# Kernel tuning notes

Measured on AMD Instinct MI355X. Metric: run time of the kernel, lower is better.

The kernel has to match this reference:

```python
import jax, jax.numpy as jnp
import numpy as np

B, S, D, H = 2, 2048, 2048, 16
HD = D // H  # 128


def setup_inputs() -> dict:
    key = jax.random.key(0)
    ks = jax.random.split(key, 7)
    x = jax.random.normal(ks[0], (B, S, D), jnp.float32)
    # 4 tree-position components per token (e.g. depth/branch coordinates)
    pos = jax.random.uniform(ks[1], (B, S, 4), jnp.float32, 0.0, 64.0)
    # tree/causal additive mask: 0 where attending is allowed, -1e9 otherwise
    causal = jnp.where(jnp.tril(jnp.ones((S, S), bool)), 0.0, -1e9).astype(jnp.float32)
    mask = jnp.broadcast_to(causal, (B, S, S))
    scale = D ** -0.5
    wq = jax.random.normal(ks[2], (D, D), jnp.float32) * scale
    wk = jax.random.normal(ks[3], (D, D), jnp.float32) * scale
    wv = jax.random.normal(ks[4], (D, D), jnp.float32) * scale
    wo = jax.random.normal(ks[5], (D, D), jnp.float32) * scale
    return {"x": x, "pos": pos, "mask": mask, "wq": wq, "wk": wk, "wv": wv, "wo": wo}


def reference(x, pos, mask, wq, wk, wv, wo):
    b, s, d = x.shape
    hd = HD
    # theta_of_dims: 1/10000^(arange(0,hd,8)[:hd//8]/hd) -> [hd//8]
    theta = 1.0 / (10000.0 ** (jnp.arange(0, hd, 8)[: hd // 8].astype(jnp.float32) / hd))
    q = (x @ wq.T).reshape(b, s, H, hd)
    k = (x @ wk.T).reshape(b, s, H, hd)
    v = (x @ wv.T).reshape(b, s, H, hd)
    # freqs: [b, s, hd//8, 4] flattened to [b, s, 1, hd//2]
    freqs = jnp.einsum('bij,k->bikj', pos, theta).reshape(b, s, 1, hd // 2)
    cos, sin = jnp.cos(freqs), jnp.sin(freqs)

    def rope(t):
        tr, ti = t[..., 0::2], t[..., 1::2]  # complex pairs (even=real, odd=imag)
        out_r = tr * cos - ti * sin
        out_i = tr * sin + ti * cos
        return jnp.stack([out_r, out_i], axis=-1).reshape(t.shape)

    q, k = rope(q), rope(k)
    scores = jnp.einsum('bqhd,bkhd->bhqk', q, k) / np.float32(np.sqrt(hd))
    scores = scores + mask[:, None, :, :]
    attn = jax.nn.softmax(scores, axis=-1)
    out = jnp.einsum('bhqk,bkhd->bqhd', attn, v).reshape(b, s, d)
    return out @ wo.T
```

## Files before the change

### kernel.cpp

```cpp
#include <hip/hip_runtime.h>
#include <cstdint>
#include <type_traits>

typedef __attribute__((ext_vector_type(8))) short short8;
typedef __attribute__((ext_vector_type(4))) float floatx4;

#define NB 2
#define NS 2048
#define ND 2048
#define NH 16
#define NHD 128

__device__ __forceinline__ float b2f(short s) {
  unsigned u = ((unsigned)(unsigned short)s) << 16;
  return __builtin_bit_cast(float, u);
}
__device__ __forceinline__ short f2b(float f) {
  unsigned u = __builtin_bit_cast(unsigned, f);
  unsigned r = (u + 0x7fffu + ((u >> 16) & 1u)) >> 16;
  return (short)(unsigned short)r;
}

__global__ void cast_all(const float* __restrict__ x, const float* __restrict__ wq,
                         const float* __restrict__ wk, const float* __restrict__ wv,
                         const float* __restrict__ wo, short* __restrict__ dst) {
  const int i = blockIdx.x * blockDim.x + threadIdx.x;
  const float* src;
  int off;
  if (i < 2097152) { src = x;  off = i; }
  else if (i < 3145728) { src = wq; off = i - 2097152; }
  else if (i < 4194304) { src = wk; off = i - 3145728; }
  else if (i < 5242880) { src = wv; off = i - 4194304; }
  else { src = wo; off = i - 5242880; }
  float4 v = ((const float4*)src)[off];
  short4 o;
  o.x = f2b(v.x); o.y = f2b(v.y); o.z = f2b(v.z); o.w = f2b(v.w);
  ((short4*)dst)[i] = o;
}

__device__ __forceinline__ void gld_lds16(const void* g, void* l) {
  __builtin_amdgcn_global_load_lds((const __attribute__((address_space(1))) void*)g,
                                   (__attribute__((address_space(3))) void*)l,
                                   16, 0, 0);
}

__global__ __launch_bounds__(256) void qkv_gemm(const short* __restrict__ A,
                                                const short* __restrict__ Bt,
                                                short* __restrict__ Qh,
                                                short* __restrict__ Kh,
                                                short* __restrict__ vlin) {
  constexpr int K = 2048;
  __shared__ short As[128 * 64];
  __shared__ short Bs[128 * 64];
  const int m0 = blockIdx.y * 128, n0 = blockIdx.x * 128;
  const int which = n0 >> 11;
  const int nl0 = n0 & 2047;
  const int t = threadIdx.x;
  const int wave = t >> 6, lane = t & 63, l15 = lane & 15, quad = lane >> 4;
  const int wm = (wave >> 1) * 64, wn = (wave & 1) * 64;

  floatx4 acc[4][4] = {};

  const int srow = t >> 3;
  const int scol = (t & 7) ^ (srow & 7);
  const short* Ag = A + (long)(m0 + srow) * K + scol * 8;
  const short* Bg = Bt + (long)(n0 + srow) * K + scol * 8;
  char* AsB = (char*)As;
  char* BsB = (char*)Bs;
  const int ldsOff = wave * 1024;

  for (int kt = 0; kt < K; kt += 64) {
#pragma unroll
    for (int i = 0; i < 4; ++i) {
      gld_lds16(Ag + kt + (long)(32 * i) * K, AsB + ldsOff + i * 4096);
      gld_lds16(Bg + kt + (long)(32 * i) * K, BsB + ldsOff + i * 4096);
    }
    __syncthreads();

#pragma unroll
    for (int half = 0; half < 2; ++half) {
      short8 a[4], b[4];
#pragma unroll
      for (int mi = 0; mi < 4; ++mi) {
        const int rr = wm + mi * 16 + l15;
        a[mi] = *(const short8*)&As[rr * 64 + (((half << 2) | quad) ^ (rr & 7)) * 8];
      }
#pragma unroll
      for (int ni = 0; ni < 4; ++ni) {
        const int rr = wn + ni * 16 + l15;
        b[ni] = *(const short8*)&Bs[rr * 64 + (((half << 2) | quad) ^ (rr & 7)) * 8];
      }
#pragma unroll
      for (int mi = 0; mi < 4; ++mi)
#pragma unroll
        for (int ni = 0; ni < 4; ++ni)
          acc[mi][ni] = __builtin_amdgcn_mfma_f32_16x16x32_bf16(a[mi], b[ni], acc[mi][ni], 0, 0, 0);
    }
    __syncthreads();
  }

  short* headDst = (which == 0) ? Qh : Kh;
#pragma unroll
  for (int mi = 0; mi < 4; ++mi) {
#pragma unroll
    for (int ni = 0; ni < 4; ++ni) {
#pragma unroll
      for (int r = 0; r < 4; ++r) {
        const int row = m0 + wm + mi * 16 + quad * 4 + r;
        const int col = nl0 + wn + ni * 16 + l15;
        const short v = f2b(acc[mi][ni][r]);
        if (which == 2) {
          vlin[(long)row * 2048 + col] = v;
        } else {
          const int bb = row >> 11, s = row & 2047, h = col >> 7, hd = col & 127;
          headDst[(((long)(bb * 16 + h) * 2048) + s) * 128 + hd] = v;
        }
      }
    }
  }
}

__global__ __launch_bounds__(256) void gemm_out(const short* __restrict__ A,
                                                const short* __restrict__ Bt,
                                                float* __restrict__ Cout) {
  constexpr int K = 2048, N = 2048;
  __shared__ short As[128 * 64];
  __shared__ short Bs[128 * 64];
  const int m0 = blockIdx.y * 128, n0 = blockIdx.x * 128;
  const int t = threadIdx.x;
  const int wave = t >> 6, lane = t & 63, l15 = lane & 15, quad = lane >> 4;
  const int wm = (wave >> 1) * 64, wn = (wave & 1) * 64;

  floatx4 acc[4][4] = {};

  const int srow = t >> 3;
  const int scol = (t & 7) ^ (srow & 7);
  const short* Ag = A + (long)(m0 + srow) * K + scol * 8;
  const short* Bg = Bt + (long)(n0 + srow) * K + scol * 8;
  char* AsB = (char*)As;
  char* BsB = (char*)Bs;
  const int ldsOff = wave * 1024;

  for (int kt = 0; kt < K; kt += 64) {
#pragma unroll
    for (int i = 0; i < 4; ++i) {
      gld_lds16(Ag + kt + (long)(32 * i) * K, AsB + ldsOff + i * 4096);
      gld_lds16(Bg + kt + (long)(32 * i) * K, BsB + ldsOff + i * 4096);
    }
    __syncthreads();

#pragma unroll
    for (int half = 0; half < 2; ++half) {
      short8 a[4], b[4];
#pragma unroll
      for (int mi = 0; mi < 4; ++mi) {
        const int rr = wm + mi * 16 + l15;
        a[mi] = *(const short8*)&As[rr * 64 + (((half << 2) | quad) ^ (rr & 7)) * 8];
      }
#pragma unroll
      for (int ni = 0; ni < 4; ++ni) {
        const int rr = wn + ni * 16 + l15;
        b[ni] = *(const short8*)&Bs[rr * 64 + (((half << 2) | quad) ^ (rr & 7)) * 8];
      }
#pragma unroll
      for (int mi = 0; mi < 4; ++mi)
#pragma unroll
        for (int ni = 0; ni < 4; ++ni)
          acc[mi][ni] = __builtin_amdgcn_mfma_f32_16x16x32_bf16(a[mi], b[ni], acc[mi][ni], 0, 0, 0);
    }
    __syncthreads();
  }

#pragma unroll
  for (int mi = 0; mi < 4; ++mi)
#pragma unroll
    for (int ni = 0; ni < 4; ++ni)
#pragma unroll
      for (int r = 0; r < 4; ++r) {
        const int row = m0 + wm + mi * 16 + quad * 4 + r;
        const int col = n0 + wn + ni * 16 + l15;
        Cout[(long)row * N + col] = acc[mi][ni][r];
      }
}

__global__ __launch_bounds__(256) void rope_vtrans(short* __restrict__ Qh,
                                                   short* __restrict__ Kh,
                                                   const float* __restrict__ pos,
                                                   const short* __restrict__ v_lin,
                                                   short* __restrict__ Vt) {
  __shared__ short tile[64 * 72];
  const int bx = blockIdx.x;
  if (bx < 4096) {
    const int tid = bx * 256 + threadIdx.x;
    const int kk = tid & 15;
    const int h = (tid >> 4) & 15;
    const int token = tid >> 8;
    const int bb = token >> 11, s = token & 2047;
    const float4 p4 = ((const float4*)pos)[token];
    const float pv[4] = {p4.x, p4.y, p4.z, p4.w};
    const float theta = exp2f(-(float)kk * 0.8304820237218406f);
    const long base = (((long)(bb * 16 + h)) * 2048 + s) * 128 + kk * 8;
    short8 q8 = *(short8*)(Qh + base);
    short8 k8 = *(short8*)(Kh + base);
    short8 qo, ko;
#pragma unroll
    for (int jj = 0; jj < 4; ++jj) {
      const float fr = pv[jj] * theta;
      float sn, c;
      __sincosf(fr, &sn, &c);
      {
        const float tr = b2f(q8[2 * jj]), ti = b2f(q8[2 * jj + 1]);
        qo[2 * jj] = f2b(tr * c - ti * sn);
        qo[2 * jj + 1] = f2b(tr * sn + ti * c);
      }
      {
        const float tr = b2f(k8[2 * jj]), ti = b2f(k8[2 * jj + 1]);
        ko[2 * jj] = f2b(tr * c - ti * sn);
        ko[2 * jj + 1] = f2b(tr * sn + ti * c);
      }
    }
    *(short8*)(Qh + base) = qo;
    *(short8*)(Kh + base) = ko;
  } else {
    const int b2 = bx - 4096;
    const int s0 = (b2 & 31) * 64;
    const int hd0 = ((b2 >> 5) & 1) * 64;
    const int bh = b2 >> 6;
    const int bb = bh >> 4, h = bh & 15;
    const int t = threadIdx.x;
#pragma unroll
    for (int i = 0; i < 2; ++i) {
      const int ch = t + i * 256;
      const int r = ch >> 3, c = ch & 7;
      *(short8*)&tile[r * 72 + c * 8] =
          *(const short8*)(v_lin + (long)(bb * 2048 + s0 + r) * 2048 + h * 128 + hd0 + c * 8);
    }
    __syncthreads();
#pragma unroll
    for (int i = 0; i < 2; ++i) {
      const int ch = t + i * 256;
      const int r2 = ch >> 3, c2 = ch & 7;
      short8 o;
#pragma unroll
      for (int u = 0; u < 8; ++u) o[u] = tile[(c2 * 8 + u) * 72 + r2];
      *(short8*)(Vt + ((long)(bh * 128 + hd0 + r2)) * 2048 + s0 + c2 * 8) = o;
    }
  }
}

__global__ __launch_bounds__(256, 2) void flash(const short* __restrict__ Qh,
                                                const short* __restrict__ Kh,
                                                const short* __restrict__ Vt,
                                                short* __restrict__ ao) {
  __shared__ short Ks[64 * 136];
  __shared__ short Vts[128 * 68];
  __shared__ short Ps[4 * 32 * 72];
  const int a = blockIdx.x;
  const int bh = blockIdx.y;
  const int t = threadIdx.x, wave = t >> 6, lane = t & 63, l15 = lane & 15, quad = lane >> 4;
  const int sqb[2] = {a * 64, (31 - a) * 64};
  const int lastkt0 = a, lastkt1 = 31 - a;

  const short* Qbase = Qh + (long)bh * 2048 * 128;
  short8 aq[2][4];
#pragma unroll
  for (int rb = 0; rb < 2; ++rb)
#pragma unroll
    for (int ks = 0; ks < 4; ++ks)
      aq[rb][ks] = *(const short8*)(Qbase + (long)(sqb[rb] + wave * 16 + l15) * 128 + ks * 32 + quad * 8);

  const short* KgBase = Kh + (long)bh * 2048 * 128;
  const short* VgBase = Vt + (long)bh * 128 * 2048;

  short8 kreg[4], vreg[4];
#pragma unroll
  for (int i = 0; i < 4; ++i) {
    const int ch = t + i * 256;
    kreg[i] = *(const short8*)(KgBase + (long)(ch >> 4) * 128 + (ch & 15) * 8);
    vreg[i] = *(const short8*)(VgBase + (long)(ch >> 3) * 2048 + (ch & 7) * 8);
  }

  float l_part[2][4] = {};
  floatx4 acc_o[2][8] = {};
  const float CEXP = 0.12751745f;

  for (int kt = 0; kt <= lastkt1; ++kt) {
    const int k0 = kt * 64;
    if (kt > 0) __syncthreads();

#pragma unroll
    for (int i = 0; i < 4; ++i) {
      const int ch = t + i * 256;
      *(short8*)&Ks[(ch >> 4) * 136 + (ch & 15) * 8] = kreg[i];
      *(short8*)&Vts[(ch >> 3) * 68 + (ch & 7) * 8] = vreg[i];
    }
    __syncthreads();

    if (kt < lastkt1) {
      const short* Kg = KgBase + (long)(k0 + 64) * 128;
      const short* Vg = VgBase + (k0 + 64);
#pragma unroll
      for (int i = 0; i < 4; ++i) {
        const int ch = t + i * 256;
        kreg[i] = *(const short8*)(Kg + (long)(ch >> 4) * 128 + (ch & 15) * 8);
        vreg[i] = *(const short8*)(Vg + (long)(ch >> 3) * 2048 + (ch & 7) * 8);
      }
    }

    const bool dgf[2] = {kt == lastkt0, kt == lastkt1};

    auto step = [&](auto DO0C) {
      constexpr bool DO0 = decltype(DO0C)::value;
      floatx4 accs[2][4] = {};
#pragma unroll
      for (int ks = 0; ks < 4; ++ks) {
#pragma unroll
        for (int ni = 0; ni < 4; ++ni) {
          const short8 bk = *(const short8*)&Ks[(ni * 16 + l15) * 136 + ks * 32 + quad * 8];
          accs[1][ni] = __builtin_amdgcn_mfma_f32_16x16x32_bf16(aq[1][ks], bk, accs[1][ni], 0, 0, 0);
          if (DO0)
            accs[0][ni] = __builtin_amdgcn_mfma_f32_16x16x32_bf16(aq[0][ks], bk, accs[0][ni], 0, 0, 0);
        }
      }
#pragma unroll
      for (int rb = 0; rb < 2; ++rb) {
        if (rb == 0 && !DO0) continue;
        const bool dg = dgf[rb];
#pragma unroll
        for (int r = 0; r < 4; ++r) {
          const int qrow = sqb[rb] + wave * 16 + quad * 4 + r;
#pragma unroll
          for (int ni = 0; ni < 4; ++ni) {
            float e = exp2f(accs[rb][ni][r] * CEXP);
            if (dg && (k0 + ni * 16 + l15) > qrow) e = 0.f;
            Ps[wave * 2304 + (rb * 16 + quad * 4 + r) * 72 + ni * 16 + l15] = f2b(e);
            l_part[rb][r] += e;
          }
        }
      }
#pragma unroll
      for (int ks2 = 0; ks2 < 2; ++ks2) {
        short8 ap1 = *(const short8*)&Ps[wave * 2304 + (16 + l15) * 72 + ks2 * 32 + quad * 8];
        short8 ap0;
        if (DO0) ap0 = *(const short8*)&Ps[wave * 2304 + l15 * 72 + ks2 * 32 + quad * 8];
#pragma unroll
        for (int nh = 0; nh < 8; ++nh) {
          const short8 bv = *(const short8*)&Vts[(nh * 16 + l15) * 68 + ks2 * 32 + quad * 8];
          acc_o[1][nh] = __builtin_amdgcn_mfma_f32_16x16x32_bf16(ap1, bv, acc_o[1][nh], 0, 0, 0);
          if (DO0)
            acc_o[0][nh] = __builtin_amdgcn_mfma_f32_16x16x32_bf16(ap0, bv, acc_o[0][nh], 0, 0, 0);
        }
      }
    };

    if (kt <= lastkt0)
      step(std::integral_constant<bool, true>{});
    else
      step(std::integral_constant<bool, false>{});
  }

  const int bb = bh >> 4, h = bh & 15;
#pragma unroll
  for (int rb = 0; rb < 2; ++rb) {
#pragma unroll
    for (int r = 0; r < 4; ++r) {
      float rs = l_part[rb][r];
#pragma unroll
      for (int mm = 8; mm >= 1; mm >>= 1) rs += __shfl_xor(rs, mm, 16);
      const float inv = 1.0f / rs;
      const int s = sqb[rb] + wave * 16 + quad * 4 + r;
      const long rowbase = ((long)(bb * 2048 + s)) * 2048 + h * 128;
#pragma unroll
      for (int nh = 0; nh < 8; ++nh) ao[rowbase + nh * 16 + l15] = f2b(acc_o[rb][nh][r] * inv);
    }
  }
}

extern "C" void kernel_launch(void* const* d_in, const int* in_sizes, int n_in,
                              void* d_out, int out_size, void* d_ws, size_t ws_size,
                              hipStream_t stream) {
  const float* x = (const float*)d_in[0];
  const float* pos = (const float*)d_in[1];
  const float* wq = (const float*)d_in[3];
  const float* wk = (const float*)d_in[4];
  const float* wv = (const float*)d_in[5];
  const float* wo = (const float*)d_in[6];
  float* out = (float*)d_out;

  char* ws = (char*)d_ws;
  const size_t MB = 1024 * 1024;
  short* xb    = (short*)(ws + 0);
  short* wqkvb = (short*)(ws + 16 * MB);
  short* wob   = (short*)(ws + 40 * MB);
  short* Qh    = (short*)(ws + 48 * MB);
  short* Kh    = (short*)(ws + 64 * MB);
  short* Vt    = (short*)(ws + 80 * MB);
  short* vlin  = (short*)(ws + 96 * MB);
  short* ao    = (short*)(ws + 96 * MB);

  cast_all<<<24576, 256, 0, stream>>>(x, wq, wk, wv, wo, xb);

  qkv_gemm<<<dim3(48, 32), 256, 0, stream>>>(xb, wqkvb, Qh, Kh, vlin);

  rope_vtrans<<<6144, 256, 0, stream>>>(Qh, Kh, pos, vlin, Vt);

  flash<<<dim3(16, 32), 256, 0, stream>>>(Qh, Kh, Vt, ao);

  gemm_out<<<dim3(16, 32), 256, 0, stream>>>(ao, wob, out);
}
```

Baseline: 411.2 us.

## Rework QKV GEMM into 256x256 double-buffered tiles with interleaved prefetch and setprio

The QKV projection GEMM moves from 128x128 tiles with 4 waves to 256x256 tiles with 8 waves and double-buffered LDS. The next k-tile's global-to-LDS loads are issued in the middle of the MFMA phases, and a block-index swizzle is added to improve L2 reuse. s_setprio is raised around the MFMA sections in both the GEMM and the flash-attention kernel so matrix work gets issue priority. This is meant to hide load latency and raise reuse per tile. In exchange the kernel uses 128KB of LDS and a larger accumulator set, and launches fewer blocks.

Measured after the change: 449.5 us. +9.3%, slower.

```diff
diff --git a/kernel.cpp b/kernel.cpp
--- a/kernel.cpp
+++ b/kernel.cpp
@@ -44,22 +44,56 @@
                                    16, 0, 0);
 }
 
-__global__ __launch_bounds__(256) void qkv_gemm(const short* __restrict__ A,
-                                                const short* __restrict__ Bt,
-                                                short* __restrict__ Qh,
-                                                short* __restrict__ Kh,
-                                                short* __restrict__ vlin) {
-  constexpr int K = 2048;
-  __shared__ short As[128 * 64];
-  __shared__ short Bs[128 * 64];
-  const int m0 = blockIdx.y * 128, n0 = blockIdx.x * 128;
+#define QKV_STAGE_A                                                                  \
+  if (T + 1 < NT) {                                                                  \
+    _Pragma("unroll") for (int i = 0; i < 4; ++i)                                    \
+        gld_lds16(Ag + knext + (long)(i * 64) * K, AsB + nbOff + wOff + i * 8192);   \
+  }
+#define QKV_STAGE_B                                                                  \
+  if (T + 1 < NT) {                                                                  \
+    _Pragma("unroll") for (int i = 0; i < 4; ++i)                                    \
+        gld_lds16(Bg + knext + (long)(i * 64) * K, BsB + nbOff + wOff + i * 8192);   \
+  }
+#define QKV_VMW asm volatile("s_waitcnt vmcnt(0)" ::: "memory");
+
+#define QKV_PHASE(MI0, MI1, STAGE, VMW)                                              \
+  {                                                                                  \
+    short8 a0k0 = lda(MI0, 0), a0k1 = lda(MI0, 1);                                   \
+    short8 a1k0 = lda(MI1, 0), a1k1 = lda(MI1, 1);                                   \
+    STAGE                                                                            \
+    VMW                                                                              \
+    __builtin_amdgcn_s_barrier();                                                    \
+    __builtin_amdgcn_s_setprio(1);                                                   \
+    _Pragma("unroll") for (int ni = 0; ni < 4; ++ni) {                               \
+      acc[MI0][ni] = __builtin_amdgcn_mfma_f32_16x16x32_bf16(a0k0, bfr[ni][0], acc[MI0][ni], 0, 0, 0); \
+      acc[MI1][ni] = __builtin_amdgcn_mfma_f32_16x16x32_bf16(a1k0, bfr[ni][0], acc[MI1][ni], 0, 0, 0); \
+    }                                                                                \
+    _Pragma("unroll") for (int ni = 0; ni < 4; ++ni) {                               \
+      acc[MI0][ni] = __builtin_amdgcn_mfma_f32_16x16x32_bf16(a0k1, bfr[ni][1], acc[MI0][ni], 0, 0, 0); \
+      acc[MI1][ni] = __builtin_amdgcn_mfma_f32_16x16x32_bf16(a1k1, bfr[ni][1], acc[MI1][ni], 0, 0, 0); \
+    }                                                                                \
+    __builtin_amdgcn_s_setprio(0);                                                   \
+    __builtin_amdgcn_s_barrier();                                                    \
+  }
+
+__global__ __launch_bounds__(512, 2) void qkv_gemm(const short* __restrict__ A,
+                                                   const short* __restrict__ Bt,
+                                                   short* __restrict__ Qh,
+                                                   short* __restrict__ Kh,
+                                                   short* __restrict__ vlin) {
+  constexpr int K = 2048, NT = K / 64;
+  __shared__ short As[2][256 * 64];
+  __shared__ short Bs[2][256 * 64];
+  const int flat = blockIdx.y * 24 + blockIdx.x;
+  const int sw = (flat & 7) * 48 + (flat >> 3);
+  const int m0 = (sw / 24) * 256, n0 = (sw % 24) * 256;
   const int which = n0 >> 11;
   const int nl0 = n0 & 2047;
   const int t = threadIdx.x;
   const int wave = t >> 6, lane = t & 63, l15 = lane & 15, quad = lane >> 4;
-  const int wm = (wave >> 1) * 64, wn = (wave & 1) * 64;
-
-  floatx4 acc[4][4] = {};
+  const int wr = wave >> 2, wc = wave & 3;
+
+  floatx4 acc[8][4] = {};
 
   const int srow = t >> 3;
   const int scol = (t & 7) ^ (srow & 7);
@@ -67,53 +101,57 @@
   const short* Bg = Bt + (long)(n0 + srow) * K + scol * 8;
   char* AsB = (char*)As;
   char* BsB = (char*)Bs;
-  const int ldsOff = wave * 1024;
-
-  for (int kt = 0; kt < K; kt += 64) {
-#pragma unroll
-    for (int i = 0; i < 4; ++i) {
-      gld_lds16(Ag + kt + (long)(32 * i) * K, AsB + ldsOff + i * 4096);
-      gld_lds16(Bg + kt + (long)(32 * i) * K, BsB + ldsOff + i * 4096);
-    }
-    __syncthreads();
-
-#pragma unroll
-    for (int half = 0; half < 2; ++half) {
-      short8 a[4], b[4];
-#pragma unroll
-      for (int mi = 0; mi < 4; ++mi) {
-        const int rr = wm + mi * 16 + l15;
-        a[mi] = *(const short8*)&As[rr * 64 + (((half << 2) | quad) ^ (rr & 7)) * 8];
-      }
-#pragma unroll
-      for (int ni = 0; ni < 4; ++ni) {
-        const int rr = wn + ni * 16 + l15;
-        b[ni] = *(const short8*)&Bs[rr * 64 + (((half << 2) | quad) ^ (rr & 7)) * 8];
-      }
-#pragma unroll
-      for (int mi = 0; mi < 4; ++mi)
-#pragma unroll
-        for (int ni = 0; ni < 4; ++ni)
-          acc[mi][ni] = __builtin_amdgcn_mfma_f32_16x16x32_bf16(a[mi], b[ni], acc[mi][ni], 0, 0, 0);
-    }
-    __syncthreads();
+  const int wOff = wave * 1024;
+
+#pragma unroll
+  for (int i = 0; i < 4; ++i) gld_lds16(Ag + (long)(i * 64) * K, AsB + wOff + i * 8192);
+#pragma unroll
+  for (int i = 0; i < 4; ++i) gld_lds16(Bg + (long)(i * 64) * K, BsB + wOff + i * 8192);
+  asm volatile("s_waitcnt vmcnt(0)" ::: "memory");
+  __builtin_amdgcn_s_barrier();
+
+  for (int T = 0; T < NT; ++T) {
+    const int bb = T & 1;
+    const int nbOff = (bb ^ 1) * 32768;
+    const long knext = (long)(T + 1) * 64;
+    const short* Asb = &As[bb][0];
+    const short* Bsb = &Bs[bb][0];
+
+    auto lda = [&](int mi, int kk) -> short8 {
+      const int rr = wr * 128 + mi * 16 + l15;
+      return *(const short8*)&Asb[rr * 64 + (((kk << 2) | quad) ^ (rr & 7)) * 8];
+    };
+
+    short8 bfr[4][2];
+#pragma unroll
+    for (int ni = 0; ni < 4; ++ni)
+#pragma unroll
+      for (int kk = 0; kk < 2; ++kk) {
+        const int rr = wc * 64 + ni * 16 + l15;
+        bfr[ni][kk] = *(const short8*)&Bsb[rr * 64 + (((kk << 2) | quad) ^ (rr & 7)) * 8];
+      }
+
+    QKV_PHASE(0, 1, QKV_STAGE_A, )
+    QKV_PHASE(2, 3, QKV_STAGE_B, )
+    QKV_PHASE(4, 5, , )
+    QKV_PHASE(6, 7, , QKV_VMW)
   }
 
   short* headDst = (which == 0) ? Qh : Kh;
 #pragma unroll
-  for (int mi = 0; mi < 4; ++mi) {
+  for (int mi = 0; mi < 8; ++mi) {
 #pragma unroll
     for (int ni = 0; ni < 4; ++ni) {
 #pragma unroll
       for (int r = 0; r < 4; ++r) {
-        const int row = m0 + wm + mi * 16 + quad * 4 + r;
-        const int col = nl0 + wn + ni * 16 + l15;
+        const int row = m0 + wr * 128 + mi * 16 + quad * 4 + r;
+        const int col = nl0 + wc * 64 + ni * 16 + l15;
         const short v = f2b(acc[mi][ni][r]);
         if (which == 2) {
           vlin[(long)row * 2048 + col] = v;
         } else {
-          const int bb = row >> 11, s = row & 2047, h = col >> 7, hd = col & 127;
-          headDst[(((long)(bb * 16 + h) * 2048) + s) * 128 + hd] = v;
+          const int bb2 = row >> 11, s = row & 2047, h = col >> 7, hd = col & 127;
+          headDst[(((long)(bb2 * 16 + h) * 2048) + s) * 128 + hd] = v;
         }
       }
     }
@@ -312,6 +350,7 @@
     auto step = [&](auto DO0C) {
       constexpr bool DO0 = decltype(DO0C)::value;
       floatx4 accs[2][4] = {};
+      __builtin_amdgcn_s_setprio(1);
 #pragma unroll
       for (int ks = 0; ks < 4; ++ks) {
 #pragma unroll
@@ -322,6 +361,7 @@
             accs[0][ni] = __builtin_amdgcn_mfma_f32_16x16x32_bf16(aq[0][ks], bk, accs[0][ni], 0, 0, 0);
         }
       }
+      __builtin_amdgcn_s_setprio(0);
 #pragma unroll
       for (int rb = 0; rb < 2; ++rb) {
         if (rb == 0 && !DO0) continue;
@@ -338,6 +378,7 @@
           }
         }
       }
+      __builtin_amdgcn_s_setprio(1);
 #pragma unroll
       for (int ks2 = 0; ks2 < 2; ++ks2) {
         short8 ap1 = *(const short8*)&Ps[wave * 2304 + (16 + l15) * 72 + ks2 * 32 + quad * 8];
@@ -351,6 +392,7 @@
             acc_o[0][nh] = __builtin_amdgcn_mfma_f32_16x16x32_bf16(ap0, bv, acc_o[0][nh], 0, 0, 0);
         }
       }
+      __builtin_amdgcn_s_setprio(0);
     };
 
     if (kt <= lastkt0)
@@ -400,7 +442,7 @@
 
   cast_all<<<24576, 256, 0, stream>>>(x, wq, wk, wv, wo, xb);
 
-  qkv_gemm<<<dim3(48, 32), 256, 0, stream>>>(xb, wqkvb, Qh, Kh, vlin);
+  qkv_gemm<<<dim3(24, 16), 512, 0, stream>>>(xb, wqkvb, Qh, Kh, vlin);
 
   rope_vtrans<<<6144, 256, 0, stream>>>(Qh, Kh, pos, vlin, Vt);
 
```

## Split paired causal query tiles into one tile per block with priority hints

Applied to the files above, without the earlier changes.

The flash kernel no longer pairs query tile a with tile 31-a in one block. Each block now handles a single 64-row query tile, giving twice as many blocks with unequal causal work. Halving per-thread Q and accumulator state lets launch bounds rise to three blocks per CU. s_setprio raises wave priority around the MFMA sections. The cost is that each K/V tile load now serves only one query tile instead of two, which doubles LDS staging traffic per unit of compute, and load balance relies on the hardware scheduler.

Result: slower. 468.8 us (+14.0%).

```diff
diff --git a/kernel.cpp b/kernel.cpp
--- a/kernel.cpp
+++ b/kernel.cpp
@@ -248,26 +248,24 @@
   }
 }
 
-__global__ __launch_bounds__(256, 2) void flash(const short* __restrict__ Qh,
+__global__ __launch_bounds__(256, 3) void flash(const short* __restrict__ Qh,
                                                 const short* __restrict__ Kh,
                                                 const short* __restrict__ Vt,
                                                 short* __restrict__ ao) {
   __shared__ short Ks[64 * 136];
   __shared__ short Vts[128 * 68];
-  __shared__ short Ps[4 * 32 * 72];
-  const int a = blockIdx.x;
+  __shared__ short Ps[4 * 16 * 72];
+  const int qt = blockIdx.x;
   const int bh = blockIdx.y;
   const int t = threadIdx.x, wave = t >> 6, lane = t & 63, l15 = lane & 15, quad = lane >> 4;
-  const int sqb[2] = {a * 64, (31 - a) * 64};
-  const int lastkt0 = a, lastkt1 = 31 - a;
+  const int sqb = qt * 64;
+  const int lastkt = qt;
 
   const short* Qbase = Qh + (long)bh * 2048 * 128;
-  short8 aq[2][4];
-#pragma unroll
-  for (int rb = 0; rb < 2; ++rb)
-#pragma unroll
-    for (int ks = 0; ks < 4; ++ks)
-      aq[rb][ks] = *(const short8*)(Qbase + (long)(sqb[rb] + wave * 16 + l15) * 128 + ks * 32 + quad * 8);
+  short8 aq[4];
+#pragma unroll
+  for (int ks = 0; ks < 4; ++ks)
+    aq[ks] = *(const short8*)(Qbase + (long)(sqb + wave * 16 + l15) * 128 + ks * 32 + quad * 8);
 
   const short* KgBase = Kh + (long)bh * 2048 * 128;
   const short* VgBase = Vt + (long)bh * 128 * 2048;
@@ -280,11 +278,11 @@
     vreg[i] = *(const short8*)(VgBase + (long)(ch >> 3) * 2048 + (ch & 7) * 8);
   }
 
-  float l_part[2][4] = {};
-  floatx4 acc_o[2][8] = {};
+  float l_part[4] = {};
+  floatx4 acc_o[8] = {};
   const float CEXP = 0.12751745f;
 
-  for (int kt = 0; kt <= lastkt1; ++kt) {
+  for (int kt = 0; kt <= lastkt; ++kt) {
     const int k0 = kt * 64;
     if (kt > 0) __syncthreads();
 
@@ -296,7 +294,7 @@
     }
     __syncthreads();
 
-    if (kt < lastkt1) {
+    if (kt < lastkt) {
       const short* Kg = KgBase + (long)(k0 + 64) * 128;
       const short* Vg = VgBase + (k0 + 64);
 #pragma unroll
@@ -307,72 +305,53 @@
       }
     }
 
-    const bool dgf[2] = {kt == lastkt0, kt == lastkt1};
-
-    auto step = [&](auto DO0C) {
-      constexpr bool DO0 = decltype(DO0C)::value;
-      floatx4 accs[2][4] = {};
-#pragma unroll
-      for (int ks = 0; ks < 4; ++ks) {
-#pragma unroll
-        for (int ni = 0; ni < 4; ++ni) {
-          const short8 bk = *(const short8*)&Ks[(ni * 16 + l15) * 136 + ks * 32 + quad * 8];
-          accs[1][ni] = __builtin_amdgcn_mfma_f32_16x16x32_bf16(aq[1][ks], bk, accs[1][ni], 0, 0, 0);
-          if (DO0)
-            accs[0][ni] = __builtin_amdgcn_mfma_f32_16x16x32_bf16(aq[0][ks], bk, accs[0][ni], 0, 0, 0);
-        }
-      }
-#pragma unroll
-      for (int rb = 0; rb < 2; ++rb) {
-        if (rb == 0 && !DO0) continue;
-        const bool dg = dgf[rb];
-#pragma unroll
-        for (int r = 0; r < 4; ++r) {
-          const int qrow = sqb[rb] + wave * 16 + quad * 4 + r;
-#pragma unroll
-          for (int ni = 0; ni < 4; ++ni) {
-            float e = exp2f(accs[rb][ni][r] * CEXP);
-            if (dg && (k0 + ni * 16 + l15) > qrow) e = 0.f;
-            Ps[wave * 2304 + (rb * 16 + quad * 4 + r) * 72 + ni * 16 + l15] = f2b(e);
-            l_part[rb][r] += e;
-          }
-        }
-      }
-#pragma unroll
-      for (int ks2 = 0; ks2 < 2; ++ks2) {
-        short8 ap1 = *(const short8*)&Ps[wave * 2304 + (16 + l15) * 72 + ks2 * 32 + quad * 8];
-        short8 ap0;
-        if (DO0) ap0 = *(const short8*)&Ps[wave * 2304 + l15 * 72 + ks2 * 32 + quad * 8];
-#pragma unroll
-        for (int nh = 0; nh < 8; ++nh) {
-          const short8 bv = *(const short8*)&Vts[(nh * 16 + l15) * 68 + ks2 * 32 + quad * 8];
-          acc_o[1][nh] = __builtin_amdgcn_mfma_f32_16x16x32_bf16(ap1, bv, acc_o[1][nh], 0, 0, 0);
-          if (DO0)
-            acc_o[0][nh] = __builtin_amdgcn_mfma_f32_16x16x32_bf16(ap0, bv, acc_o[0][nh], 0, 0, 0);
-        }
-      }
-    };
-
-    if (kt <= lastkt0)
-      step(std::integral_constant<bool, true>{});
-    else
-      step(std::integral_constant<bool, false>{});
+    const bool dg = (kt == lastkt);
+    floatx4 accs[4] = {};
+    __builtin_amdgcn_s_setprio(1);
+#pragma unroll
+    for (int ks = 0; ks < 4; ++ks) {
+#pragma unroll
+      for (int ni = 0; ni < 4; ++ni) {
+        const short8 bk = *(const short8*)&Ks[(ni * 16 + l15) * 136 + ks * 32 + quad * 8];
+        accs[ni] = __builtin_amdgcn_mfma_f32_16x16x32_bf16(aq[ks], bk, accs[ni], 0, 0, 0);
+      }
+    }
+    __builtin_amdgcn_s_setprio(0);
+#pragma unroll
+    for (int r = 0; r < 4; ++r) {
+      const int qrow = sqb + wave * 16 + quad * 4 + r;
+#pragma unroll
+      for (int ni = 0; ni < 4; ++ni) {
+        float e = exp2f(accs[ni][r] * CEXP);
+        if (dg && (k0 + ni * 16 + l15) > qrow) e = 0.f;
+        Ps[wave * 1152 + (quad * 4 + r) * 72 + ni * 16 + l15] = f2b(e);
+        l_part[r] += e;
+      }
+    }
+    __builtin_amdgcn_s_setprio(1);
+#pragma unroll
+    for (int ks2 = 0; ks2 < 2; ++ks2) {
+      const short8 ap = *(const short8*)&Ps[wave * 1152 + l15 * 72 + ks2 * 32 + quad * 8];
+#pragma unroll
+      for (int nh = 0; nh < 8; ++nh) {
+        const short8 bv = *(const short8*)&Vts[(nh * 16 + l15) * 68 + ks2 * 32 + quad * 8];
+        acc_o[nh] = __builtin_amdgcn_mfma_f32_16x16x32_bf16(ap, bv, acc_o[nh], 0, 0, 0);
+      }
+    }
+    __builtin_amdgcn_s_setprio(0);
   }
 
   const int bb = bh >> 4, h = bh & 15;
 #pragma unroll
-  for (int rb = 0; rb < 2; ++rb) {
-#pragma unroll
-    for (int r = 0; r < 4; ++r) {
-      float rs = l_part[rb][r];
-#pragma unroll
-      for (int mm = 8; mm >= 1; mm >>= 1) rs += __shfl_xor(rs, mm, 16);
-      const float inv = 1.0f / rs;
-      const int s = sqb[rb] + wave * 16 + quad * 4 + r;
-      const long rowbase = ((long)(bb * 2048 + s)) * 2048 + h * 128;
-#pragma unroll
-      for (int nh = 0; nh < 8; ++nh) ao[rowbase + nh * 16 + l15] = f2b(acc_o[rb][nh][r] * inv);
-    }
+  for (int r = 0; r < 4; ++r) {
+    float rs = l_part[r];
+#pragma unroll
+    for (int mm = 8; mm >= 1; mm >>= 1) rs += __shfl_xor(rs, mm, 16);
+    const float inv = 1.0f / rs;
+    const int s = sqb + wave * 16 + quad * 4 + r;
+    const long rowbase = ((long)(bb * 2048 + s)) * 2048 + h * 128;
+#pragma unroll
+    for (int nh = 0; nh < 8; ++nh) ao[rowbase + nh * 16 + l15] = f2b(acc_o[nh][r] * inv);
   }
 }
 
@@ -404,7 +383,7 @@
 
   rope_vtrans<<<6144, 256, 0, stream>>>(Qh, Kh, pos, vlin, Vt);
 
-  flash<<<dim3(16, 32), 256, 0, stream>>>(Qh, Kh, Vt, ao);
+  flash<<<dim3(32, 32), 256, 0, stream>>>(Qh, Kh, Vt, ao);
 
   gemm_out<<<dim3(16, 32), 256, 0, stream>>>(ao, wob, out);
 }
```
